# Kernel optimization log

Hardware: AMD Instinct MI355X
Metric: run time of the kernel (lower is better)

## Reference

```python
import jax, jax.numpy as jnp
import numpy as np

MESSAGE_PASSES = 3  # constants.message_passes
F_NODE = 64   # hidden_node_features
F_EDGE = 16   # n_edge_features
M_MSG = 64    # message_size
OUT_DIM = 128
B, N = 8, 256
EDGE_DENSITY = 0.1


def setup_inputs() -> dict:
    key = jax.random.key(0)
    ks = jax.random.split(key, 12)
    nodes = jax.random.normal(ks[0], (B, N, F_NODE), dtype=jnp.float32)
    # sparse positive edge features: rand * bernoulli connectivity (avg degree ~ N*density)
    raw = jax.random.uniform(ks[1], (B, N, N, F_EDGE), dtype=jnp.float32)
    conn = (jax.random.uniform(ks[2], (B, N, N)) < EDGE_DENSITY).astype(jnp.float32)
    edges = raw * conn[..., None]
    s = 0.05
    return {
        "nodes": nodes,
        "edges": edges,
        # message MLP: cat(neighbour, edge) -> message_size
        "W_msg": jax.random.normal(ks[3], (F_NODE + F_EDGE, M_MSG), dtype=jnp.float32) * s,
        "b_msg": jnp.zeros((M_MSG,), dtype=jnp.float32),
        # GRU cell (input=message_size, hidden=F_NODE), gates [r|z|n]
        "W_i": jax.random.normal(ks[4], (M_MSG, 3 * F_NODE), dtype=jnp.float32) * s,
        "W_h": jax.random.normal(ks[5], (F_NODE, 3 * F_NODE), dtype=jnp.float32) * s,
        "b_i": jnp.zeros((3 * F_NODE,), dtype=jnp.float32),
        "b_h": jnp.zeros((3 * F_NODE,), dtype=jnp.float32),
        # gated readout
        "W_g": jax.random.normal(ks[6], (2 * F_NODE, OUT_DIM), dtype=jnp.float32) * s,
        "b_g": jnp.zeros((OUT_DIM,), dtype=jnp.float32),
        "W_e": jax.random.normal(ks[7], (F_NODE, OUT_DIM), dtype=jnp.float32) * s,
        "b_e": jnp.zeros((OUT_DIM,), dtype=jnp.float32),
    }


def reference(nodes, edges, W_msg, b_msg, W_i, W_h, b_i, b_h, W_g, b_g, W_e, b_e):
    # adjacency[b,i,j] != 0  <=>  edge (i<-j) exists (original: edges.sum(3).nonzero)
    adjacency = edges.sum(axis=-1)                                   # (B,N,N)
    nbr_mask = (adjacency != 0).astype(nodes.dtype)                  # (B,N,N)
    node_mask = (adjacency.sum(axis=-1) != 0)                        # (B,N) bool
    node_mask_f = node_mask.astype(nodes.dtype)

    h = nodes                                                        # hidden_nodes init = nodes
    b, n, f = nodes.shape
    for _ in range(MESSAGE_PASSES):
        # message_terms over all (node i, neighbour j) pairs; masked sum == padded-gather sum
        nghb = jnp.broadcast_to(h[:, None, :, :], (b, n, n, f))      # (B,N,N,F) neighbour feats
        feat = jnp.concatenate([nghb, edges], axis=-1)               # (B,N,N,F+E)
        terms = jax.nn.relu(feat @ W_msg + b_msg)                    # (B,N,N,M)
        messages = jnp.einsum('bijm,bij->bim', terms, nbr_mask)      # summation aggregation
        # GRU cell update
        gi = messages @ W_i + b_i                                    # (B,N,3F)
        gh = h @ W_h + b_h
        ir, iz, inn = jnp.split(gi, 3, axis=-1)
        hr, hz, hn = jnp.split(gh, 3, axis=-1)
        r = jax.nn.sigmoid(ir + hr)
        z = jax.nn.sigmoid(iz + hz)
        ng = jnp.tanh(inn + r * hn)
        h_new = (1.0 - z) * ng + z * h
        # only nodes with nonzero degree are scattered back (original indexes node_batch idc)
        h = jnp.where(node_mask[..., None], h_new, h)

    # gated readout: sum_i mask_i * sigmoid(g([h_i, x_i])) * e(h_i)
    gate = jax.nn.sigmoid(jnp.concatenate([h, nodes], axis=-1) @ W_g + b_g)  # (B,N,OUT)
    emb = h @ W_e + b_e                                                      # (B,N,OUT)
    out = jnp.einsum('bno,bn->bo', gate * emb, node_mask_f)                  # (B,OUT)
    return out
```

## Files before the change

kernel.cpp:

```cpp
#include <hip/hip_runtime.h>

#define BB 8
#define NN 256
#define FF 64
#define EE 16
#define MM 64
#define G3 192
#define OUTD 128
#define ROWS (BB*NN)
#define MAXD 64

__device__ __forceinline__ float sigmoidf_(float x) {
    return 1.0f / (1.0f + __expf(-x));
}

__global__ __launch_bounds__(512, 4) void k_prep2(
    const float* __restrict__ nodes, const float* __restrict__ edges,
    const float* __restrict__ Wmsg, const float* __restrict__ bmsg,
    int* __restrict__ deg, int* __restrict__ nbr, float* __restrict__ gef,
    float* __restrict__ h, float* __restrict__ hn_out, float* __restrict__ out)
{
    const int r0  = blockIdx.x * 2;
    const int tid = threadIdx.x;
    const int w   = tid >> 6;
    const int lane = tid & 63;

    __shared__ int   sdeg[2];
    __shared__ float swm[FF][MM];
    __shared__ float part[8][MM];
    __shared__ float shold[2][FF];

    if (blockIdx.x == 0) { out[tid] = 0.0f; out[tid + 512] = 0.0f; }
    if (tid < 2) sdeg[tid] = 0;
    if (tid < 2 * FF) {
        int r = tid >> 6;
        float v = nodes[(size_t)(r0 + r) * FF + (tid & 63)];
        shold[r][tid & 63] = v;
        h[(size_t)(r0 + r) * FF + (tid & 63)] = v;
    }
    for (int i = tid; i < FF * MM; i += 512) swm[i >> 6][i & 63] = Wmsg[i];
    __syncthreads();

    const float4* base4 = (const float4*)(edges + (size_t)r0 * NN * EE);
    #pragma unroll
    for (int it = 0; it < 4; ++it) {
        int p  = it * 512 + tid;
        float4 v = base4[p];
        int e  = it * 128 + (tid >> 2);
        int rr = e >> 8;
        int j  = e & 255;
        int q  = lane & 3;
        float s4 = v.x + v.y + v.z + v.w;
        s4 += __shfl_xor(s4, 1);
        s4 += __shfl_xor(s4, 2);
        bool pred = (s4 != 0.0f);
        unsigned long long mk = __ballot(pred && (q == 0));
        int cnt = __popcll(mk);
        int base = 0;
        if (lane == 0) base = atomicAdd(&sdeg[rr], cnt);
        base = __shfl(base, 0);
        int slot = base + __popcll(mk & ((1ull << (lane & ~3)) - 1ull));
        if (pred && slot < MAXD) {
            ((float4*)(gef + ((size_t)(r0 + rr) * MAXD + slot) * EE))[q] = v;
            if (q == 0) nbr[(r0 + rr) * MAXD + slot] = j;
        }
    }
    __syncthreads();
    if (tid < 2) {
        int t = sdeg[tid]; t = t < MAXD ? t : MAXD;
        deg[r0 + tid] = t;
    }

    {
        int r = w >> 2, kq = w & 3;
        float p = 0.0f;
        #pragma unroll
        for (int kk = 0; kk < 16; ++kk) {
            int k = kq * 16 + kk;
            p += shold[r][k] * swm[k][lane];
        }
        part[w][lane] = p;
    }
    __syncthreads();
    if (tid < 2 * MM) {
        int r = tid >> 6, tt = tid & 63;
        hn_out[(size_t)(r0 + r) * MM + tt] = bmsg[tt]
            + part[r*4+0][tt] + part[r*4+1][tt] + part[r*4+2][tt] + part[r*4+3][tt];
    }
}

__global__ __launch_bounds__(512, 4) void k_p12(
    const float* __restrict__ Wmsg, const float* __restrict__ bmsg,
    const float* __restrict__ Wi, const float* __restrict__ Wh,
    const float* __restrict__ bi, const float* __restrict__ bh,
    const float* __restrict__ nodes,
    const float* __restrict__ Wg, const float* __restrict__ bg,
    const float* __restrict__ We, const float* __restrict__ be,
    const int* __restrict__ deg, const int* __restrict__ nbr,
    const float* __restrict__ gef,
    const float* __restrict__ hn_in, float* __restrict__ hn_out,
    float* __restrict__ h, float* __restrict__ out, int last)
{
    const int r0  = blockIdx.x * 2;
    const int b   = r0 >> 8;
    const int tid = threadIdx.x;
    const int w   = tid >> 6;
    const int lane = tid & 63;

    __shared__ int   snbr[2][MAXD];
    __shared__ int   sdeg[2];
    __shared__ __align__(16) float efeat[2][MAXD][EE];
    __shared__ float part[8][MM];
    __shared__ float smsg[2][MM];
    __shared__ float shold[2][FF];
    __shared__ float sx[2][FF];
    __shared__ float gI[2][3][FF], gH[2][3][FF];
    __shared__ float shnew[2][FF];
    __shared__ float sg[2][OUTD], se[2][OUTD];

    const int d0 = deg[r0], d1 = deg[r0 + 1];
    if (tid == 0) { sdeg[0] = d0; sdeg[1] = d1; }

    if (tid < 2 * MAXD) {
        int r = tid >> 6;
        snbr[r][tid & 63] = nbr[(r0 + r) * MAXD + (tid & 63)];
    }
    if (tid < 2 * FF) {
        int r = tid >> 6;
        shold[r][tid & 63] = h[(size_t)(r0 + r) * FF + (tid & 63)];
    }
    if (last && tid >= 2 * FF && tid < 4 * FF) {
        int r = (tid >> 6) & 1;
        sx[r][tid & 63] = nodes[(size_t)(r0 + r) * FF + (tid & 63)];
    }
    {
        const float4* g0 = (const float4*)(gef + (size_t)r0 * MAXD * EE);
        const float4* g1 = (const float4*)(gef + (size_t)(r0 + 1) * MAXD * EE);
        for (int i = tid; i < d0 * 4; i += 512) ((float4*)efeat[0])[i] = g0[i];
        for (int i = tid; i < d1 * 4; i += 512) ((float4*)efeat[1])[i] = g1[i];
    }
    float we[EE];
    #pragma unroll
    for (int k = 0; k < EE; ++k) we[k] = Wmsg[(FF + k) * MM + lane];
    __syncthreads();

    {
        int r = w >> 2, sub = w & 3;
        int d = sdeg[r];
        const float* hb = hn_in + (size_t)b * NN * MM;
        float acc = 0.0f;
        for (int s = sub; s < d; s += 4) {
            int j = snbr[r][s];
            float term = hb[j * MM + lane];
            #pragma unroll
            for (int k = 0; k < EE; ++k) term += efeat[r][s][k] * we[k];
            acc += fmaxf(term, 0.0f);
        }
        part[w][lane] = acc;
    }
    __syncthreads();
    if ((w & 3) == 0) {
        int r = w >> 2;
        smsg[r][lane] = part[w][lane] + part[w + 1][lane]
                      + part[w + 2][lane] + part[w + 3][lane];
    }
    __syncthreads();

    if (w < 3) {
        float a0 = bi[w * FF + lane], a1 = a0;
        #pragma unroll 4
        for (int k = 0; k < FF; ++k) {
            float wgt = Wi[k * G3 + w * FF + lane];
            a0 += smsg[0][k] * wgt;
            a1 += smsg[1][k] * wgt;
        }
        gI[0][w][lane] = a0; gI[1][w][lane] = a1;
    } else if (w < 6) {
        int g = w - 3;
        float a0 = bh[g * FF + lane], a1 = a0;
        #pragma unroll 4
        for (int k = 0; k < FF; ++k) {
            float wgt = Wh[k * G3 + g * FF + lane];
            a0 += shold[0][k] * wgt;
            a1 += shold[1][k] * wgt;
        }
        gH[0][g][lane] = a0; gH[1][g][lane] = a1;
    }
    __syncthreads();

    if (tid < 2 * FF) {
        int r = tid >> 6, tt = tid & 63;
        float rr = sigmoidf_(gI[r][0][tt] + gH[r][0][tt]);
        float zz = sigmoidf_(gI[r][1][tt] + gH[r][1][tt]);
        float ng = tanhf(gI[r][2][tt] + rr * gH[r][2][tt]);
        float hold = shold[r][tt];
        float hnew = (1.0f - zz) * ng + zz * hold;
        if (sdeg[r] == 0) hnew = hold;
        shnew[r][tt] = hnew;
        h[(size_t)(r0 + r) * FF + tt] = hnew;
    }
    __syncthreads();

    if (!last) {
        {
            int r = w >> 2, kq = w & 3;
            float p = 0.0f;
            #pragma unroll
            for (int kk = 0; kk < 16; ++kk) {
                int k = kq * 16 + kk;
                p += shnew[r][k] * Wmsg[k * MM + lane];
            }
            part[w][lane] = p;
        }
        __syncthreads();
        if (tid < 2 * MM) {
            int r = tid >> 6, tt = tid & 63;
            hn_out[(size_t)(r0 + r) * MM + tt] = bmsg[tt]
                + part[r*4+0][tt] + part[r*4+1][tt] + part[r*4+2][tt] + part[r*4+3][tt];
        }
    } else {
        int grp = tid >> 7, o = tid & 127;
        int r = grp >> 1, kind = grp & 1;
        if (kind == 0) {
            float g = bg[o];
            #pragma unroll 4
            for (int k = 0; k < FF; ++k) g += shnew[r][k] * Wg[k * OUTD + o];
            #pragma unroll 4
            for (int k = 0; k < FF; ++k) g += sx[r][k] * Wg[(FF + k) * OUTD + o];
            sg[r][o] = g;
        } else {
            float e = be[o];
            #pragma unroll 4
            for (int k = 0; k < FF; ++k) e += shnew[r][k] * We[k * OUTD + o];
            se[r][o] = e;
        }
        __syncthreads();
        if (tid < OUTD) {
            float v0 = (sdeg[0] != 0) ? sigmoidf_(sg[0][tid]) * se[0][tid] : 0.0f;
            float v1 = (sdeg[1] != 0) ? sigmoidf_(sg[1][tid]) * se[1][tid] : 0.0f;
            atomicAdd(&out[b * OUTD + tid], v0 + v1);
        }
    }
}

extern "C" void kernel_launch(void* const* d_in, const int* in_sizes, int n_in,
                              void* d_out, int out_size, void* d_ws, size_t ws_size,
                              hipStream_t stream) {
    const float* nodes = (const float*)d_in[0];
    const float* edges = (const float*)d_in[1];
    const float* Wmsg  = (const float*)d_in[2];
    const float* bmsg  = (const float*)d_in[3];
    const float* Wi    = (const float*)d_in[4];
    const float* Wh    = (const float*)d_in[5];
    const float* bi    = (const float*)d_in[6];
    const float* bh    = (const float*)d_in[7];
    const float* Wg    = (const float*)d_in[8];
    const float* bg    = (const float*)d_in[9];
    const float* We    = (const float*)d_in[10];
    const float* be    = (const float*)d_in[11];
    float* out = (float*)d_out;
    char* ws = (char*)d_ws;

    int*   deg  = (int*)ws;
    int*   nbr  = (int*)(ws + 8192);
    float* gef  = (float*)(ws + 8192 + (size_t)ROWS * MAXD * 4);
    float* h    = gef + (size_t)ROWS * MAXD * EE;
    float* hnA  = h   + (size_t)ROWS * FF;
    float* hnB  = hnA + (size_t)ROWS * MM;

    k_prep2<<<ROWS/2, 512, 0, stream>>>(nodes, edges, Wmsg, bmsg,
                                        deg, nbr, gef, h, hnA, out);
    k_p12<<<ROWS/2, 512, 0, stream>>>(Wmsg, bmsg, Wi, Wh, bi, bh,
                                      nodes, Wg, bg, We, be, deg, nbr, gef,
                                      hnA, hnB, h, out, 0);
    k_p12<<<ROWS/2, 512, 0, stream>>>(Wmsg, bmsg, Wi, Wh, bi, bh,
                                      nodes, Wg, bg, We, be, deg, nbr, gef,
                                      hnB, hnA, h, out, 0);
    k_p12<<<ROWS/2, 512, 0, stream>>>(Wmsg, bmsg, Wi, Wh, bi, bh,
                                      nodes, Wg, bg, We, be, deg, nbr, gef,
                                      hnA, hnB, h, out, 1);
}
```

Baseline: 145.9 us.

## Batch edge loads, drop h init copy, vectorize edge-feature dot

```diff
diff --git a/kernel.cpp b/kernel.cpp
--- a/kernel.cpp
+++ b/kernel.cpp
@@ -18,7 +18,7 @@
     const float* __restrict__ nodes, const float* __restrict__ edges,
     const float* __restrict__ Wmsg, const float* __restrict__ bmsg,
     int* __restrict__ deg, int* __restrict__ nbr, float* __restrict__ gef,
-    float* __restrict__ h, float* __restrict__ hn_out, float* __restrict__ out)
+    float* __restrict__ hn_out, float* __restrict__ out)
 {
     const int r0  = blockIdx.x * 2;
     const int tid = threadIdx.x;
@@ -34,38 +34,41 @@
     if (tid < 2) sdeg[tid] = 0;
     if (tid < 2 * FF) {
         int r = tid >> 6;
-        float v = nodes[(size_t)(r0 + r) * FF + (tid & 63)];
-        shold[r][tid & 63] = v;
-        h[(size_t)(r0 + r) * FF + (tid & 63)] = v;
-    }
-    for (int i = tid; i < FF * MM; i += 512) swm[i >> 6][i & 63] = Wmsg[i];
+        shold[r][tid & 63] = nodes[(size_t)(r0 + r) * FF + (tid & 63)];
+    }
     __syncthreads();
 
     const float4* base4 = (const float4*)(edges + (size_t)r0 * NN * EE);
+    float4 v[4];
+    bool pred[4];
+    #pragma unroll
+    for (int it = 0; it < 4; ++it) v[it] = base4[it * 512 + tid];
     #pragma unroll
     for (int it = 0; it < 4; ++it) {
-        int p  = it * 512 + tid;
-        float4 v = base4[p];
+        float s4 = v[it].x + v[it].y + v[it].z + v[it].w;
+        s4 += __shfl_xor(s4, 1);
+        s4 += __shfl_xor(s4, 2);
+        pred[it] = (s4 != 0.0f);
+    }
+
+    const int q = lane & 3;
+    #pragma unroll
+    for (int it = 0; it < 4; ++it) {
         int e  = it * 128 + (tid >> 2);
         int rr = e >> 8;
         int j  = e & 255;
-        int q  = lane & 3;
-        float s4 = v.x + v.y + v.z + v.w;
-        s4 += __shfl_xor(s4, 1);
-        s4 += __shfl_xor(s4, 2);
-        bool pred = (s4 != 0.0f);
-        unsigned long long mk = __ballot(pred && (q == 0));
-        int cnt = __popcll(mk);
-        int base = 0;
-        if (lane == 0) base = atomicAdd(&sdeg[rr], cnt);
-        base = __shfl(base, 0);
-        int slot = base + __popcll(mk & ((1ull << (lane & ~3)) - 1ull));
-        if (pred && slot < MAXD) {
-            ((float4*)(gef + ((size_t)(r0 + rr) * MAXD + slot) * EE))[q] = v;
+        int slot = 0;
+        if (pred[it] && q == 0) slot = atomicAdd(&sdeg[rr], 1);
+        slot = __shfl(slot, lane & ~3);
+        if (pred[it] && slot < MAXD) {
+            ((float4*)(gef + ((size_t)(r0 + rr) * MAXD + slot) * EE))[q] = v[it];
             if (q == 0) nbr[(r0 + rr) * MAXD + slot] = j;
         }
     }
-    __syncthreads();
+
+    for (int i = tid; i < FF * MM; i += 512) swm[i >> 6][i & 63] = Wmsg[i];
+    __syncthreads();
+
     if (tid < 2) {
         int t = sdeg[tid]; t = t < MAXD ? t : MAXD;
         deg[r0 + tid] = t;
@@ -97,7 +100,7 @@
     const float* __restrict__ Wg, const float* __restrict__ bg,
     const float* __restrict__ We, const float* __restrict__ be,
     const int* __restrict__ deg, const int* __restrict__ nbr,
-    const float* __restrict__ gef,
+    const float* __restrict__ gef, const float* __restrict__ hsrc,
     const float* __restrict__ hn_in, float* __restrict__ hn_out,
     float* __restrict__ h, float* __restrict__ out, int last)
 {
@@ -127,7 +130,7 @@
     }
     if (tid < 2 * FF) {
         int r = tid >> 6;
-        shold[r][tid & 63] = h[(size_t)(r0 + r) * FF + (tid & 63)];
+        shold[r][tid & 63] = hsrc[(size_t)(r0 + r) * FF + (tid & 63)];
     }
     if (last && tid >= 2 * FF && tid < 4 * FF) {
         int r = (tid >> 6) & 1;
@@ -152,8 +155,12 @@
         for (int s = sub; s < d; s += 4) {
             int j = snbr[r][s];
             float term = hb[j * MM + lane];
-            #pragma unroll
-            for (int k = 0; k < EE; ++k) term += efeat[r][s][k] * we[k];
+            const float4* e4 = (const float4*)efeat[r][s];
+            float4 e0 = e4[0], e1 = e4[1], e2 = e4[2], e3 = e4[3];
+            term += e0.x*we[0] + e0.y*we[1] + e0.z*we[2] + e0.w*we[3]
+                  + e1.x*we[4] + e1.y*we[5] + e1.z*we[6] + e1.w*we[7]
+                  + e2.x*we[8] + e2.y*we[9] + e2.z*we[10] + e2.w*we[11]
+                  + e3.x*we[12] + e3.y*we[13] + e3.z*we[14] + e3.w*we[15];
             acc += fmaxf(term, 0.0f);
         }
         part[w][lane] = acc;
@@ -197,7 +204,7 @@
         float hnew = (1.0f - zz) * ng + zz * hold;
         if (sdeg[r] == 0) hnew = hold;
         shnew[r][tt] = hnew;
-        h[(size_t)(r0 + r) * FF + tt] = hnew;
+        if (!last) h[(size_t)(r0 + r) * FF + tt] = hnew;
     }
     __syncthreads();
 
@@ -269,14 +276,14 @@
     float* hnB  = hnA + (size_t)ROWS * MM;
 
     k_prep2<<<ROWS/2, 512, 0, stream>>>(nodes, edges, Wmsg, bmsg,
-                                        deg, nbr, gef, h, hnA, out);
+                                        deg, nbr, gef, hnA, out);
     k_p12<<<ROWS/2, 512, 0, stream>>>(Wmsg, bmsg, Wi, Wh, bi, bh,
                                       nodes, Wg, bg, We, be, deg, nbr, gef,
-                                      hnA, hnB, h, out, 0);
+                                      nodes, hnA, hnB, h, out, 0);
     k_p12<<<ROWS/2, 512, 0, stream>>>(Wmsg, bmsg, Wi, Wh, bi, bh,
                                       nodes, Wg, bg, We, be, deg, nbr, gef,
-                                      hnB, hnA, h, out, 0);
+                                      h, hnB, hnA, h, out, 0);
     k_p12<<<ROWS/2, 512, 0, stream>>>(Wmsg, bmsg, Wi, Wh, bi, bh,
                                       nodes, Wg, bg, We, be, deg, nbr, gef,
-                                      hnA, hnB, h, out, 1);
-}
+                                      h, hnA, hnB, h, out, 1);
+}
```

Result: no change. 145.0 us (median of 2 runs) (-0.6%).
